# Kernel tuning notes

Hardware: AMD Instinct MI355X
Metric: run time of the kernel (lower is better)

The kernel has to match this reference:

```python
import jax, jax.numpy as jnp
import numpy as np

BIG = 1e30  # stand-in for +inf at DP boundaries (never selected by min)


def setup_inputs() -> dict:
    key = jax.random.key(0)
    kx, kp = jax.random.split(key)
    B, D, T = 32, 16, 1024        # batch, channels (d_patts), stream length
    P, L = 64, 32                 # n_patts, l_patts
    x = jax.random.normal(kx, (B, D, T), dtype=jnp.float32)
    patts = jax.random.normal(kp, (P, D, L), dtype=jnp.float32)
    rho = 0.5
    w = float(rho ** (1.0 / L))   # self.w = rho ** (1 / l_patts)
    return {"x": x, "patts": patts, "w": w}


def _dtw(x, patts, w):
    # Weighted streaming DTW: for each pattern p and each ending time j,
    # D[i, j] = cost[i, j] + min(D[i-1, j], w*D[i, j-1], w*D[i-1, j-1])
    # with D[i, 0] = cost[i, 0] + D[i-1, 0] (first time column cumsum) and
    # cost[i, j] = ||x[:, j] - patts[:, i]||^2 (squared euclidean over channels).
    B, D, T = x.shape
    P, _, L = patts.shape
    p2 = jnp.sum(patts * patts, axis=1)                       # (P, L)

    def cost_at(xj):                                          # xj: (B, D)
        x2 = jnp.sum(xj * xj, axis=1)                         # (B,)
        xp = jnp.einsum('bd,pdl->bpl', xj, patts)             # (B, P, L)
        return x2[:, None, None] + p2[None] - 2.0 * xp        # (B, P, L)

    # first time column
    col0 = jnp.cumsum(cost_at(x[:, :, 0]), axis=-1)           # (B, P, L)

    def step(prev, xj):
        cost = cost_at(xj)                                    # (B, P, L)
        prev_up = jnp.concatenate(
            [jnp.full_like(prev[..., :1], BIG), prev[..., :-1]], axis=-1)
        m = w * jnp.minimum(prev, prev_up)                    # (B, P, L)

        def inner(new_im1, cm):                               # scan along pattern axis
            c_i, m_i = cm
            new_i = c_i + jnp.minimum(new_im1, m_i)
            return new_i, new_i

        _, new = jax.lax.scan(
            inner, jnp.full((B, P), BIG, cost.dtype),
            (jnp.moveaxis(cost, -1, 0), jnp.moveaxis(m, -1, 0)))
        new_col = jnp.moveaxis(new, 0, -1)                    # (B, P, L)
        return new_col, new_col[..., -1]                      # emit full-pattern match cost

    xs = jnp.moveaxis(x[:, :, 1:], -1, 0)                     # (T-1, B, D)
    _, rest = jax.lax.scan(step, col0, xs)                    # (T-1, B, P)
    dtw = jnp.concatenate([col0[None, ..., -1], rest], axis=0)  # (T, B, P)
    return jnp.moveaxis(dtw, 0, -1)                           # (B, P, T)


def reference(x, patts, w):
    return jnp.sqrt(_dtw(x, patts, w))
```

## Files before the change

### kernel.cpp

```cpp
#include <hip/hip_runtime.h>
#include <math.h>

#define B_ 32
#define D_ 16
#define T_ 1024
#define P_ 64
#define L_ 32
#define KB 524288.0f

typedef short short8 __attribute__((ext_vector_type(8)));
typedef float f32x4 __attribute__((ext_vector_type(4)));
typedef unsigned short ushort_t;

template<int CTRL, int ROW_MASK, bool BC>
__device__ __forceinline__ float dpp_mov(float old_, float src) {
  int o = __builtin_bit_cast(int, old_);
  int s = __builtin_bit_cast(int, src);
  int r = __builtin_amdgcn_update_dpp(o, s, CTRL, ROW_MASK, 0xf, BC);
  return __builtin_bit_cast(float, r);
}

__device__ __forceinline__ float scan_sum32(float v) {
  v += dpp_mov<0x111, 0xf, true>(0.f, v);
  v += dpp_mov<0x112, 0xf, true>(0.f, v);
  v += dpp_mov<0x114, 0xf, true>(0.f, v);
  v += dpp_mov<0x118, 0xf, true>(0.f, v);
  v += dpp_mov<0x142, 0xa, false>(0.f, v);
  return v;
}

__device__ __forceinline__ float scan_max32(float v) {
  asm("s_nop 1\n\t"
      "v_max_f32_dpp %0, %0, %0 row_shr:1 row_mask:0xf bank_mask:0xf\n\t"
      "s_nop 1\n\t"
      "v_max_f32_dpp %0, %0, %0 row_shr:2 row_mask:0xf bank_mask:0xf\n\t"
      "s_nop 1\n\t"
      "v_max_f32_dpp %0, %0, %0 row_shr:4 row_mask:0xf bank_mask:0xf\n\t"
      "s_nop 1\n\t"
      "v_max_f32_dpp %0, %0, %0 row_shr:8 row_mask:0xf bank_mask:0xf\n\t"
      "s_nop 1\n\t"
      "v_max_f32_dpp %0, %0, %0 row_bcast:15 row_mask:0xa bank_mask:0xf"
      : "+v"(v));
  return v;
}

__device__ __forceinline__ ushort_t f2bf(float f) {
  unsigned u = __builtin_bit_cast(unsigned, f);
  return (ushort_t)((u + 0x7FFFu + ((u >> 16) & 1u)) >> 16);
}
__device__ __forceinline__ float bf2f(ushort_t h) {
  unsigned u = ((unsigned)h) << 16;
  return __builtin_bit_cast(float, u);
}

__global__ __launch_bounds__(256) void prep_fused(
    const float* __restrict__ x, const float* __restrict__ patts,
    ushort_t* __restrict__ xA, ushort_t* __restrict__ pB) {
  const int bid = blockIdx.x;
  if (bid < 128) {
    int gid = bid * 256 + threadIdx.x;
    int b = gid >> 10, t = gid & 1023;
    float x2 = 0.f;
    ushort_t o[32];
#pragma unroll
    for (int d = 0; d < 16; ++d) {
      float v = x[((b * 16 + d) << 10) + t];
      x2 = fmaf(v, v, x2);
      o[d] = f2bf(v);
    }
    o[16] = 0x3F80; o[17] = 0x3F80;
    ushort_t hi = f2bf(x2);
    o[18] = hi;
    o[19] = f2bf(x2 - bf2f(hi));
#pragma unroll
    for (int d = 20; d < 32; ++d) o[d] = 0;
    uint4* dst = (uint4*)(xA + (size_t)gid * 32);
#pragma unroll
    for (int q = 0; q < 4; ++q) {
      const ushort_t* s = o + q * 8;
      uint4 u;
      u.x = (unsigned)s[0] | ((unsigned)s[1] << 16);
      u.y = (unsigned)s[2] | ((unsigned)s[3] << 16);
      u.z = (unsigned)s[4] | ((unsigned)s[5] << 16);
      u.w = (unsigned)s[6] | ((unsigned)s[7] << 16);
      dst[q] = u;
    }
  } else {
    __shared__ float Ls[4][16 * 33];
    __shared__ float Lh[4][64];
    __shared__ float LP2[4][32];
    const int sub = threadIdx.x >> 6;
    const int l = threadIdx.x & 63;
    const int p = (bid - 128) * 4 + sub;
    const int half = l >> 5;
    const int m = l & 31;

    float p2acc = 0.f;
#pragma unroll
    for (int dd = 0; dd < 16; dd += 2) {
      int d = dd + half;
      float v = patts[((p * 16 + d) << 5) + m];
      p2acc = fmaf(v, v, p2acc);
      Ls[sub][d * 33 + m] = scan_sum32(v);
    }
    Lh[sub][l] = p2acc;
    __syncthreads();
    {
      float tot = Lh[sub][m] + Lh[sub][32 + m];
      float pref = scan_sum32(tot);
      if (half == 0) LP2[sub][m] = pref;
    }
    __syncthreads();

    const int n = l & 15, q = l >> 4;
#pragma unroll
    for (int iblk = 0; iblk < 2; ++iblk) {
      const int i = iblk * 16 + n;
      ushort_t o[8];
      if (q < 2) {
#pragma unroll
        for (int e = 0; e < 8; ++e)
          o[e] = f2bf(-2.f * Ls[sub][(q * 8 + e) * 33 + i]);
      } else if (q == 2) {
        float P2 = LP2[sub][i];
        ushort_t hi = f2bf(P2);
        o[0] = hi; o[1] = f2bf(P2 - bf2f(hi));
        o[2] = f2bf((float)(i + 1)); o[3] = o[2];
        o[4] = o[5] = o[6] = o[7] = 0;
      } else {
#pragma unroll
        for (int e = 0; e < 8; ++e) o[e] = 0;
      }
      uint4 u;
      u.x = (unsigned)o[0] | ((unsigned)o[1] << 16);
      u.y = (unsigned)o[2] | ((unsigned)o[3] << 16);
      u.z = (unsigned)o[4] | ((unsigned)o[5] << 16);
      u.w = (unsigned)o[6] | ((unsigned)o[7] << 16);
      ((uint4*)pB)[(p * 2 + iblk) * 64 + l] = u;
    }
  }
}

__global__ __launch_bounds__(256, 7) void dtw_kernel(
    const ushort_t* __restrict__ xA,
    const ushort_t* __restrict__ pBg,
    const float* __restrict__ wp,
    float* __restrict__ out)
{
  __shared__ float lds[4 * 1320];

  const int tid = threadIdx.x;
  const int l   = tid & 63;
  const int wid = tid >> 6;
  const int li  = l & 31;
  const int g   = l >> 5;
  const int q4  = l >> 4;
  const unsigned bx = blockIdx.x;
  const int ch   = bx % 7u;
  const unsigned rest = bx / 7u;
  const int b     = rest >> 3;
  const int pbase = (rest & 7) << 3;
  const int pA  = pbase + (wid << 1);
  const float w = wp[0];
  const float nw = -w;
  const bool l0c = (li == 0), l31 = (li == 31);

  const int S0    = 7 * ch;
  const int nT    = (ch == 6) ? 22 : 23;
  const int warmT = ch ? 16 : 0;

  const short8* pBs = (const short8*)pBg;
  short8 B00 = pBs[((pA    ) * 2 + 0) * 64 + l];
  short8 B01 = pBs[((pA    ) * 2 + 1) * 64 + l];
  short8 B10 = pBs[((pA + 1) * 2 + 0) * 64 + l];
  short8 B11 = pBs[((pA + 1) * 2 + 1) * 64 + l];

  const short8* xAs = (const short8*)xA + ((size_t)b << 12);

  short8 Aa;
  auto loadA = [&](int t) {
    Aa = xAs[((((S0 + t) << 4) + (l & 15)) << 2) + q4];
  };

  float* base = lds + wid * 1320;
  float* ldsW = base + 20 + (l & 15) * 20 + q4 * 4;
  const float* ldsR = base + 20 + g * 660 + li * 20;

  const f32x4 zk = {KB, KB, KB, KB};

  auto fill = [&]() {
    f32x4 d0 = __builtin_amdgcn_mfma_f32_16x16x32_bf16(Aa, B00, zk, 0, 0, 0);
    f32x4 d1 = __builtin_amdgcn_mfma_f32_16x16x32_bf16(Aa, B01, zk, 0, 0, 0);
    f32x4 d2 = __builtin_amdgcn_mfma_f32_16x16x32_bf16(Aa, B10, zk, 0, 0, 0);
    f32x4 d3 = __builtin_amdgcn_mfma_f32_16x16x32_bf16(Aa, B11, zk, 0, 0, 0);
    *(f32x4*)(ldsW + 0)   = d0;
    *(f32x4*)(ldsW + 320) = d1;
    *(f32x4*)(ldsW + 660) = d2;
    *(f32x4*)(ldsW + 980) = d3;
  };

  float* orow = out + (((size_t)(b * P_ + pA + g)) << 10) + (S0 << 4);
  float dcur = 0.f;

  loadA(0);
  fill();
  loadA(1);

  for (int t = 0; t < nT; ++t) {
    f32x4 s0 = *(const f32x4*)(ldsR + 0);
    f32x4 s1 = *(const f32x4*)(ldsR + 4);
    f32x4 s2 = *(const f32x4*)(ldsR + 8);
    f32x4 s3 = *(const f32x4*)(ldsR + 12);

    if (t + 1 < nT) fill();
    if (t + 2 < nT) loadA(t + 2);

    const bool first = (t == 0);
    const bool store = (t >= warmT);
    float* op = orow + (t << 4);

    float4 r0, r1, r2, r3;
#pragma unroll
    for (int k4 = 0; k4 < 4; ++k4) {
      f32x4 Sq = (k4 == 0) ? s0 : (k4 == 1) ? s1 : (k4 == 2) ? s2 : s3;
      float4 rv;
#pragma unroll
      for (int e = 0; e < 4; ++e) {
        float Zo = Sq[e];
        float zs = dpp_mov<0x138, 0xf, false>(KB, Zo);
        zs = l0c ? KB : zs;
        float a = fmaf(nw, dcur, zs);
        float c = fmaf(nw, dcur, Zo);
        float u;
        asm("s_nop 1\n\t"
            "v_max_f32_dpp %0, %1, %2 wave_shr:1 row_mask:0xf bank_mask:0xf"
            : "=&v"(u) : "v"(c), "v"(a));
        u = l0c ? a : u;
        float Mx = scan_max32(u);
        float val = Zo - Mx;
        if (first && k4 == 0 && e == 0)
          val = Zo - KB;
        dcur = val;
        if (e == 0) rv.x = val; else if (e == 1) rv.y = val;
        else if (e == 2) rv.z = val; else rv.w = val;
      }
      if (k4 == 0) r0 = rv; else if (k4 == 1) r1 = rv;
      else if (k4 == 2) r2 = rv; else r3 = rv;
    }
    if (store) {
      if (l31) {
        float4 s;
        s.x = __builtin_amdgcn_sqrtf(r0.x); s.y = __builtin_amdgcn_sqrtf(r0.y);
        s.z = __builtin_amdgcn_sqrtf(r0.z); s.w = __builtin_amdgcn_sqrtf(r0.w);
        *(float4*)(op + 0) = s;
        s.x = __builtin_amdgcn_sqrtf(r1.x); s.y = __builtin_amdgcn_sqrtf(r1.y);
        s.z = __builtin_amdgcn_sqrtf(r1.z); s.w = __builtin_amdgcn_sqrtf(r1.w);
        *(float4*)(op + 4) = s;
        s.x = __builtin_amdgcn_sqrtf(r2.x); s.y = __builtin_amdgcn_sqrtf(r2.y);
        s.z = __builtin_amdgcn_sqrtf(r2.z); s.w = __builtin_amdgcn_sqrtf(r2.w);
        *(float4*)(op + 8) = s;
        s.x = __builtin_amdgcn_sqrtf(r3.x); s.y = __builtin_amdgcn_sqrtf(r3.y);
        s.z = __builtin_amdgcn_sqrtf(r3.z); s.w = __builtin_amdgcn_sqrtf(r3.w);
        *(float4*)(op + 12) = s;
      }
    }
  }
}

extern "C" void kernel_launch(void* const* d_in, const int* in_sizes, int n_in,
                              void* d_out, int out_size, void* d_ws, size_t ws_size,
                              hipStream_t stream) {
  const float* x     = (const float*)d_in[0];
  const float* patts = (const float*)d_in[1];
  const float* w     = (const float*)d_in[2];
  float* out = (float*)d_out;

  ushort_t* xA = (ushort_t*)d_ws;
  ushort_t* pB = (ushort_t*)((char*)d_ws + (size_t)B_ * T_ * 32 * 2);

  prep_fused<<<144, 256, 0, stream>>>(x, patts, xA, pB);
  dtw_kernel<<<B_ * 8 * 7, 256, 0, stream>>>(xA, pB, w, out);
}
```

Before: 130.1 us.

## Replace max-plus prefix scan with anti-diagonal wavefront DTW recurrence

Drops the per-column DPP prefix-max scan formulation, which relied on cumulative sums and offset constants, and switches to an anti-diagonal wavefront. Each lane handles one pattern row, takes its neighbour's value via a single DPP shift per step, and reads skewed cost entries from a circular LDS buffer. The grid shrinks from 7 to 4 time chunks per (batch, pattern group), with LDS per block enlarged and occupancy hint lowered to 3. This cuts the five-stage scan per time step to one shuffle, at the cost of pipeline fill/drain steps and fewer, longer blocks.

```diff
diff --git a/kernel.cpp b/kernel.cpp
--- a/kernel.cpp
+++ b/kernel.cpp
@@ -6,7 +6,7 @@
 #define T_ 1024
 #define P_ 64
 #define L_ 32
-#define KB 524288.0f
+#define BIGV 1.0e30f
 
 typedef short short8 __attribute__((ext_vector_type(8)));
 typedef float f32x4 __attribute__((ext_vector_type(4)));
@@ -18,30 +18,6 @@
   int s = __builtin_bit_cast(int, src);
   int r = __builtin_amdgcn_update_dpp(o, s, CTRL, ROW_MASK, 0xf, BC);
   return __builtin_bit_cast(float, r);
-}
-
-__device__ __forceinline__ float scan_sum32(float v) {
-  v += dpp_mov<0x111, 0xf, true>(0.f, v);
-  v += dpp_mov<0x112, 0xf, true>(0.f, v);
-  v += dpp_mov<0x114, 0xf, true>(0.f, v);
-  v += dpp_mov<0x118, 0xf, true>(0.f, v);
-  v += dpp_mov<0x142, 0xa, false>(0.f, v);
-  return v;
-}
-
-__device__ __forceinline__ float scan_max32(float v) {
-  asm("s_nop 1\n\t"
-      "v_max_f32_dpp %0, %0, %0 row_shr:1 row_mask:0xf bank_mask:0xf\n\t"
-      "s_nop 1\n\t"
-      "v_max_f32_dpp %0, %0, %0 row_shr:2 row_mask:0xf bank_mask:0xf\n\t"
-      "s_nop 1\n\t"
-      "v_max_f32_dpp %0, %0, %0 row_shr:4 row_mask:0xf bank_mask:0xf\n\t"
-      "s_nop 1\n\t"
-      "v_max_f32_dpp %0, %0, %0 row_shr:8 row_mask:0xf bank_mask:0xf\n\t"
-      "s_nop 1\n\t"
-      "v_max_f32_dpp %0, %0, %0 row_bcast:15 row_mask:0xa bank_mask:0xf"
-      : "+v"(v));
-  return v;
 }
 
 __device__ __forceinline__ ushort_t f2bf(float f) {
@@ -101,14 +77,13 @@
       int d = dd + half;
       float v = patts[((p * 16 + d) << 5) + m];
       p2acc = fmaf(v, v, p2acc);
-      Ls[sub][d * 33 + m] = scan_sum32(v);
+      Ls[sub][d * 33 + m] = v;
     }
     Lh[sub][l] = p2acc;
     __syncthreads();
     {
       float tot = Lh[sub][m] + Lh[sub][32 + m];
-      float pref = scan_sum32(tot);
-      if (half == 0) LP2[sub][m] = pref;
+      if (half == 0) LP2[sub][m] = tot;
     }
     __syncthreads();
 
@@ -125,7 +100,7 @@
         float P2 = LP2[sub][i];
         ushort_t hi = f2bf(P2);
         o[0] = hi; o[1] = f2bf(P2 - bf2f(hi));
-        o[2] = f2bf((float)(i + 1)); o[3] = o[2];
+        o[2] = 0x3F80; o[3] = 0x3F80;
         o[4] = o[5] = o[6] = o[7] = 0;
       } else {
 #pragma unroll
@@ -141,13 +116,13 @@
   }
 }
 
-__global__ __launch_bounds__(256, 7) void dtw_kernel(
+__global__ __launch_bounds__(256, 3) void dtw_kernel(
     const ushort_t* __restrict__ xA,
     const ushort_t* __restrict__ pBg,
     const float* __restrict__ wp,
     float* __restrict__ out)
 {
-  __shared__ float lds[4 * 1320];
+  __shared__ float lds[4 * 3200];
 
   const int tid = threadIdx.x;
   const int l   = tid & 63;
@@ -156,18 +131,16 @@
   const int g   = l >> 5;
   const int q4  = l >> 4;
   const unsigned bx = blockIdx.x;
-  const int ch   = bx % 7u;
-  const unsigned rest = bx / 7u;
+  const int ch   = bx & 3u;
+  const unsigned rest = bx >> 2;
   const int b     = rest >> 3;
   const int pbase = (rest & 7) << 3;
   const int pA  = pbase + (wid << 1);
   const float w = wp[0];
-  const float nw = -w;
-  const bool l0c = (li == 0), l31 = (li == 31);
-
-  const int S0    = 7 * ch;
-  const int nT    = (ch == 6) ? 22 : 23;
-  const int warmT = ch ? 16 : 0;
+  const bool l0c = (li == 0);
+
+  const int S0    = 12 * ch;
+  const int warmU = ch ? 16 : 0;
 
   const short8* pBs = (const short8*)pBg;
   short8 B00 = pBs[((pA    ) * 2 + 0) * 64 + l];
@@ -176,92 +149,111 @@
   short8 B11 = pBs[((pA + 1) * 2 + 1) * 64 + l];
 
   const short8* xAs = (const short8*)xA + ((size_t)b << 12);
-
   short8 Aa;
   auto loadA = [&](int t) {
     Aa = xAs[((((S0 + t) << 4) + (l & 15)) << 2) + q4];
   };
 
-  float* base = lds + wid * 1320;
-  float* ldsW = base + 20 + (l & 15) * 20 + q4 * 4;
-  const float* ldsR = base + 20 + g * 660 + li * 20;
-
-  const f32x4 zk = {KB, KB, KB, KB};
-
-  auto fill = [&]() {
+  float* wbase = lds + wid * 3200;
+  const f32x4 zk = {0.f, 0.f, 0.f, 0.f};
+
+  auto fill = [&](int rs) {
+    float* wb = wbase + (l & 15) * 50 + rs * 16 + q4 * 4;
     f32x4 d0 = __builtin_amdgcn_mfma_f32_16x16x32_bf16(Aa, B00, zk, 0, 0, 0);
     f32x4 d1 = __builtin_amdgcn_mfma_f32_16x16x32_bf16(Aa, B01, zk, 0, 0, 0);
     f32x4 d2 = __builtin_amdgcn_mfma_f32_16x16x32_bf16(Aa, B10, zk, 0, 0, 0);
     f32x4 d3 = __builtin_amdgcn_mfma_f32_16x16x32_bf16(Aa, B11, zk, 0, 0, 0);
-    *(f32x4*)(ldsW + 0)   = d0;
-    *(f32x4*)(ldsW + 320) = d1;
-    *(f32x4*)(ldsW + 660) = d2;
-    *(f32x4*)(ldsW + 980) = d3;
+    float2 t2;
+    t2.x = d0[0]; t2.y = d0[1]; *(float2*)(wb + 0) = t2;
+    t2.x = d0[2]; t2.y = d0[3]; *(float2*)(wb + 2) = t2;
+    t2.x = d1[0]; t2.y = d1[1]; *(float2*)(wb + 800) = t2;
+    t2.x = d1[2]; t2.y = d1[3]; *(float2*)(wb + 802) = t2;
+    t2.x = d2[0]; t2.y = d2[1]; *(float2*)(wb + 1600) = t2;
+    t2.x = d2[2]; t2.y = d2[3]; *(float2*)(wb + 1602) = t2;
+    t2.x = d3[0]; t2.y = d3[1]; *(float2*)(wb + 2400) = t2;
+    t2.x = d3[2]; t2.y = d3[3]; *(float2*)(wb + 2402) = t2;
   };
 
+  const char* crow = (const char*)(wbase + g * 1600 + li * 50);
+
   float* orow = out + (((size_t)(b * P_ + pA + g)) << 10) + (S0 << 4);
-  float dcur = 0.f;
-
-  loadA(0);
-  fill();
-  loadA(1);
-
-  for (int t = 0; t < nT; ++t) {
-    f32x4 s0 = *(const f32x4*)(ldsR + 0);
-    f32x4 s1 = *(const f32x4*)(ldsR + 4);
-    f32x4 s2 = *(const f32x4*)(ldsR + 8);
-    f32x4 s3 = *(const f32x4*)(ldsR + 12);
-
-    if (t + 1 < nT) fill();
-    if (t + 2 < nT) loadA(t + 2);
-
-    const bool first = (t == 0);
-    const bool store = (t >= warmT);
-    float* op = orow + (t << 4);
-
-    float4 r0, r1, r2, r3;
-#pragma unroll
-    for (int k4 = 0; k4 < 4; ++k4) {
-      f32x4 Sq = (k4 == 0) ? s0 : (k4 == 1) ? s1 : (k4 == 2) ? s2 : s3;
-      float4 rv;
-#pragma unroll
-      for (int e = 0; e < 4; ++e) {
-        float Zo = Sq[e];
-        float zs = dpp_mov<0x138, 0xf, false>(KB, Zo);
-        zs = l0c ? KB : zs;
-        float a = fmaf(nw, dcur, zs);
-        float c = fmaf(nw, dcur, Zo);
-        float u;
-        asm("s_nop 1\n\t"
-            "v_max_f32_dpp %0, %1, %2 wave_shr:1 row_mask:0xf bank_mask:0xf"
-            : "=&v"(u) : "v"(c), "v"(a));
-        u = l0c ? a : u;
-        float Mx = scan_max32(u);
-        float val = Zo - Mx;
-        if (first && k4 == 0 && e == 0)
-          val = Zo - KB;
-        dcur = val;
-        if (e == 0) rv.x = val; else if (e == 1) rv.y = val;
-        else if (e == 2) rv.z = val; else rv.w = val;
-      }
-      if (k4 == 0) r0 = rv; else if (k4 == 1) r1 = rv;
-      else if (k4 == 2) r2 = rv; else r3 = rv;
-    }
-    if (store) {
-      if (l31) {
-        float4 s;
-        s.x = __builtin_amdgcn_sqrtf(r0.x); s.y = __builtin_amdgcn_sqrtf(r0.y);
-        s.z = __builtin_amdgcn_sqrtf(r0.z); s.w = __builtin_amdgcn_sqrtf(r0.w);
-        *(float4*)(op + 0) = s;
-        s.x = __builtin_amdgcn_sqrtf(r1.x); s.y = __builtin_amdgcn_sqrtf(r1.y);
-        s.z = __builtin_amdgcn_sqrtf(r1.z); s.w = __builtin_amdgcn_sqrtf(r1.w);
-        *(float4*)(op + 4) = s;
-        s.x = __builtin_amdgcn_sqrtf(r2.x); s.y = __builtin_amdgcn_sqrtf(r2.y);
-        s.z = __builtin_amdgcn_sqrtf(r2.z); s.w = __builtin_amdgcn_sqrtf(r2.w);
-        *(float4*)(op + 8) = s;
-        s.x = __builtin_amdgcn_sqrtf(r3.x); s.y = __builtin_amdgcn_sqrtf(r3.y);
-        s.z = __builtin_amdgcn_sqrtf(r3.z); s.w = __builtin_amdgcn_sqrtf(r3.w);
-        *(float4*)(op + 12) = s;
+
+  loadA(0); fill(0);
+  loadA(1); fill(1);
+  loadA(2);
+
+  float prev, sp2 = BIGV;
+  int offb = ((li == 0) ? 0 : (48 - li)) << 2;
+  {
+    float c0 = *(const float*)(crow + offb);
+    prev = l0c ? c0 : BIGV;
+    offb += 4; if (offb >= 192) offb -= 192;
+  }
+  for (int d = 1; d < 31; ++d) {
+    float c = *(const float*)(crow + offb);
+    offb += 4; if (offb >= 192) offb -= 192;
+    float sp = dpp_mov<0x138, 0xf, true>(0.f, prev);
+    sp = l0c ? BIGV : sp;
+    float u2 = fminf(prev, sp2);
+    float r  = fminf(sp, w * u2);
+    float Dv = c + r;
+    Dv = (li > d) ? BIGV : Dv;
+    sp2 = sp; prev = Dv;
+  }
+
+  int rsf = 2;
+  for (int u = 0; u < 28; ++u) {
+    if (u + 2 < 28) {
+      fill(rsf);
+      rsf = (rsf == 2) ? 0 : rsf + 1;
+    }
+    if (u + 3 < 28) loadA(u + 3);
+
+    float cv[16];
+#pragma unroll
+    for (int s = 0; s < 16; ++s) {
+      int ob = offb + 4 * s;
+      ob = (ob >= 192) ? ob - 192 : ob;
+      cv[s] = *(const float*)(crow + ob);
+    }
+    offb += 64; if (offb >= 192) offb -= 192;
+
+    float Ds[16];
+#pragma unroll
+    for (int s = 0; s < 16; ++s) {
+      float sp = dpp_mov<0x138, 0xf, true>(0.f, prev);
+      sp = l0c ? BIGV : sp;
+      float u2 = fminf(prev, sp2);
+      float r  = fminf(sp, w * u2);
+      float Dv = cv[s] + r;
+      sp2 = sp; prev = Dv;
+      Ds[s] = Dv;
+    }
+
+    if (u >= warmU) {
+      if (li == 31) {
+        float* op = orow + (u << 4);
+        float4 s4;
+        s4.x = __builtin_amdgcn_sqrtf(fmaxf(Ds[0], 0.f));
+        s4.y = __builtin_amdgcn_sqrtf(fmaxf(Ds[1], 0.f));
+        s4.z = __builtin_amdgcn_sqrtf(fmaxf(Ds[2], 0.f));
+        s4.w = __builtin_amdgcn_sqrtf(fmaxf(Ds[3], 0.f));
+        *(float4*)(op + 0) = s4;
+        s4.x = __builtin_amdgcn_sqrtf(fmaxf(Ds[4], 0.f));
+        s4.y = __builtin_amdgcn_sqrtf(fmaxf(Ds[5], 0.f));
+        s4.z = __builtin_amdgcn_sqrtf(fmaxf(Ds[6], 0.f));
+        s4.w = __builtin_amdgcn_sqrtf(fmaxf(Ds[7], 0.f));
+        *(float4*)(op + 4) = s4;
+        s4.x = __builtin_amdgcn_sqrtf(fmaxf(Ds[8], 0.f));
+        s4.y = __builtin_amdgcn_sqrtf(fmaxf(Ds[9], 0.f));
+        s4.z = __builtin_amdgcn_sqrtf(fmaxf(Ds[10], 0.f));
+        s4.w = __builtin_amdgcn_sqrtf(fmaxf(Ds[11], 0.f));
+        *(float4*)(op + 8) = s4;
+        s4.x = __builtin_amdgcn_sqrtf(fmaxf(Ds[12], 0.f));
+        s4.y = __builtin_amdgcn_sqrtf(fmaxf(Ds[13], 0.f));
+        s4.z = __builtin_amdgcn_sqrtf(fmaxf(Ds[14], 0.f));
+        s4.w = __builtin_amdgcn_sqrtf(fmaxf(Ds[15], 0.f));
+        *(float4*)(op + 12) = s4;
       }
     }
   }
@@ -279,5 +271,5 @@
   ushort_t* pB = (ushort_t*)((char*)d_ws + (size_t)B_ * T_ * 32 * 2);
 
   prep_fused<<<144, 256, 0, stream>>>(x, patts, xA, pB);
-  dtw_kernel<<<B_ * 8 * 7, 256, 0, stream>>>(xA, pB, w, out);
-}
+  dtw_kernel<<<B_ * 8 * 4, 256, 0, stream>>>(xA, pB, w, out);
+}
```

After: 117.1 us. -10.0%, faster.
